# Optimization experiments

Measured on AMD Instinct MI355X. Metric: run time of the kernel, lower is better.

Reference implementation:

```python
import jax, jax.numpy as jnp
import numpy as np

N_NODES = 50000
NEG_SLOPE = 0.2  # PyG GATConv default leaky_relu slope
EPS = 1e-16      # PyG softmax denominator epsilon


def gat_layer(x, src, dst, W, a_src, a_dst, b):
    # x: [N, F_in], W: [F_in, H, F_out], a_*: [H, F_out], b: [F_out]
    h = jnp.einsum('ni,iho->nho', x, W)                      # [N, H, O]
    alpha_src = jnp.sum(h * a_src, axis=-1)                  # [N, H]
    alpha_dst = jnp.sum(h * a_dst, axis=-1)                  # [N, H]
    e = jax.nn.leaky_relu(alpha_src[src] + alpha_dst[dst], NEG_SLOPE)  # [E, H]
    # segment softmax over incoming edges of each destination node
    m = jax.ops.segment_max(e, dst, num_segments=N_NODES)   # [N, H]
    ex = jnp.exp(e - m[dst])
    s = jax.ops.segment_sum(ex, dst, num_segments=N_NODES)  # [N, H]
    alpha = ex / (s[dst] + EPS)                              # [E, H]
    out = jax.ops.segment_sum(alpha[:, :, None] * h[src], dst, num_segments=N_NODES)  # [N, H, O]
    out = out.mean(axis=1) + b                               # concat=False -> mean over heads
    return jax.nn.relu(out)                                  # norm=Identity, dropout p=0 no-op


def setup_inputs() -> dict:
    key = jax.random.key(0)
    ks = jax.random.split(key, 12)
    d = 64
    H = 4
    E = 800000
    inp = {
        'x': jax.random.normal(ks[0], (N_NODES, d), dtype=jnp.float32),
        'edge_index': jax.random.randint(ks[1], (2, E), 0, N_NODES, dtype=jnp.int64),
        'edge_attr': jax.random.normal(ks[2], (E, 8), dtype=jnp.float32),
        'dropout_rate': 0,
    }
    sc = 1.0 / np.sqrt(d)
    for li, base in ((1, 3), (2, 7)):
        inp[f'W{li}'] = jax.random.normal(ks[base], (d, H, d), dtype=jnp.float32) * sc
        inp[f'a_src{li}'] = jax.random.normal(ks[base + 1], (H, d), dtype=jnp.float32) * sc
        inp[f'a_dst{li}'] = jax.random.normal(ks[base + 2], (H, d), dtype=jnp.float32) * sc
        inp[f'b{li}'] = jnp.zeros((d,), dtype=jnp.float32)
    return inp


def reference(x, edge_index, edge_attr, dropout_rate,
              W1, a_src1, a_dst1, b1, W2, a_src2, a_dst2, b2):
    # edge_attr unused: GATConv built without edge_dim has no lin_edge.
    src, dst = edge_index[0], edge_index[1]
    x = gat_layer(x, src, dst, W1, a_src1, a_dst1, b1)
    x = gat_layer(x, src, dst, W2, a_src2, a_dst2, b2)
    return x
```

## Files before the change

### kernel.cpp

```cpp
#include <hip/hip_runtime.h>
#include <hip/hip_bf16.h>
#include <math.h>

#define N_NODES 50000
#define NEG_SLOPE 0.2f
#define EPS_DEN 1e-16f

#define NBUCK 196
#define NBLK  512

typedef float f4v __attribute__((ext_vector_type(4)));

__global__ void __launch_bounds__(256) prep_k(
    const float* __restrict__ W, const float* __restrict__ aS,
    const float* __restrict__ aD, float* __restrict__ WaSD)
{
    int tid = threadIdx.x;
    int h = tid >> 6, i = tid & 63;
    const float* wrow = W + (size_t)i * 256 + h * 64;
    const float* as = aS + h * 64;
    const float* ad = aD + h * 64;
    float ws = 0.f, wd = 0.f;
    #pragma unroll 8
    for (int o = 0; o < 64; ++o) {
        float w = wrow[o];
        ws = fmaf(w, as[o], ws);
        wd = fmaf(w, ad[o], wd);
    }
    WaSD[i * 8 + h]     = ws;
    WaSD[i * 8 + 4 + h] = wd;
}

__global__ void __launch_bounds__(256) alpha_k(
    const float* __restrict__ x, const float* __restrict__ WaSD,
    float* __restrict__ asrc, float* __restrict__ adst, int N)
{
    __shared__ float Wl[512];
    int tid = threadIdx.x;
    Wl[tid]       = WaSD[tid];
    Wl[tid + 256] = WaSD[tid + 256];
    __syncthreads();

    int node = blockIdx.x * 64 + (tid >> 2);
    int q = tid & 3;
    if (node >= N) return;

    float pS[4] = {0.f, 0.f, 0.f, 0.f};
    float pD[4] = {0.f, 0.f, 0.f, 0.f};
    const float* xp = x + (size_t)node * 64 + q * 16;
    #pragma unroll
    for (int j = 0; j < 4; ++j) {
        float4 xv = *(const float4*)(xp + j * 4);
        float xr[4] = {xv.x, xv.y, xv.z, xv.w};
        #pragma unroll
        for (int u = 0; u < 4; ++u) {
            int i = q * 16 + j * 4 + u;
            float4 wS = *(const float4*)(Wl + i * 8);
            float4 wD = *(const float4*)(Wl + i * 8 + 4);
            pS[0] = fmaf(xr[u], wS.x, pS[0]); pS[1] = fmaf(xr[u], wS.y, pS[1]);
            pS[2] = fmaf(xr[u], wS.z, pS[2]); pS[3] = fmaf(xr[u], wS.w, pS[3]);
            pD[0] = fmaf(xr[u], wD.x, pD[0]); pD[1] = fmaf(xr[u], wD.y, pD[1]);
            pD[2] = fmaf(xr[u], wD.z, pD[2]); pD[3] = fmaf(xr[u], wD.w, pD[3]);
        }
    }
    #pragma unroll
    for (int off = 1; off <= 2; off <<= 1) {
        #pragma unroll
        for (int h = 0; h < 4; ++h) {
            pS[h] += __shfl_xor(pS[h], off);
            pD[h] += __shfl_xor(pD[h], off);
        }
    }
    if (q == 0) {
        *(float4*)(asrc + 4 * (size_t)node) = make_float4(pS[0], pS[1], pS[2], pS[3]);
        *(float4*)(adst + 4 * (size_t)node) = make_float4(pD[0], pD[1], pD[2], pD[3]);
    }
}

__global__ void __launch_bounds__(256) hist_bucket_k(
    const int* __restrict__ ei, int* __restrict__ bh, int E)
{
    __shared__ int lh[NBUCK];
    int tid = threadIdx.x;
    for (int b = tid; b < NBUCK; b += 256) lh[b] = 0;
    __syncthreads();

    const int ch = (E + NBLK - 1) / NBLK;
    const int e0 = blockIdx.x * ch;
    const int e1 = min(e0 + ch, E);
    for (int e = e0 + tid; e < e1; e += 256)
        atomicAdd(&lh[ei[E + e] >> 8], 1);
    __syncthreads();
    for (int b = tid; b < NBUCK; b += 256)
        bh[(size_t)b * NBLK + blockIdx.x] = lh[b];
}

__global__ void __launch_bounds__(64) bscan_k(
    const int* __restrict__ bh, int* __restrict__ boffL, int* __restrict__ btot)
{
    const int b = blockIdx.x;
    const int lane = threadIdx.x;
    int v[8];
    int base = b * NBLK;
    #pragma unroll
    for (int u = 0; u < 8; ++u) v[u] = bh[base + lane * 8 + u];
    int t = 0;
    #pragma unroll
    for (int u = 0; u < 8; ++u) t += v[u];
    int run = t;
    #pragma unroll
    for (int off = 1; off < 64; off <<= 1) {
        int u = __shfl_up(run, off);
        if (lane >= off) run += u;
    }
    int lane_base = run - t;
    #pragma unroll
    for (int u = 0; u < 8; ++u) {
        boffL[base + lane * 8 + u] = lane_base;
        lane_base += v[u];
    }
    if (lane == 63) btot[b] = run;
}

__global__ void __launch_bounds__(256) btot_k(
    const int* __restrict__ btot, int* __restrict__ bbase,
    int* __restrict__ row, int N, int E)
{
    __shared__ int sd[256];
    int tid = threadIdx.x;
    int v = (tid < NBUCK) ? btot[tid] : 0;
    sd[tid] = v;
    __syncthreads();
    for (int off = 1; off < 256; off <<= 1) {
        int t = (tid >= off) ? sd[tid - off] : 0;
        __syncthreads();
        sd[tid] += t;
        __syncthreads();
    }
    if (tid < NBUCK) bbase[tid] = sd[tid] - v;
    if (tid == 0) { bbase[NBUCK] = E; row[N] = E; }
}

__global__ void __launch_bounds__(256) bplace_k(
    const int* __restrict__ ei, const int* __restrict__ bbase,
    const int* __restrict__ boffL, unsigned int* __restrict__ stage, int E)
{
    __shared__ int cur[NBUCK];
    int tid = threadIdx.x;
    for (int b = tid; b < NBUCK; b += 256)
        cur[b] = bbase[b] + boffL[(size_t)b * NBLK + blockIdx.x];
    __syncthreads();

    const int ch = (E + NBLK - 1) / NBLK;
    const int e0 = blockIdx.x * ch;
    const int e1 = min(e0 + ch, E);
    for (int e = e0 + tid; e < e1; e += 256) {
        int s = ei[e];
        int d = ei[E + e];
        int pos = atomicAdd(&cur[d >> 8], 1);
        stage[pos] = (unsigned int)s | ((unsigned int)(d & 255) << 16);
    }
}

__global__ void __launch_bounds__(256) bscatter_k(
    const unsigned int* __restrict__ stage, const int* __restrict__ bbase,
    int* __restrict__ row, int* __restrict__ psrc, int N)
{
    __shared__ int cnt[256];
    __shared__ int sd[256];
    __shared__ int cur[256];
    const int b = blockIdx.x;
    const int tid = threadIdx.x;
    const int nb0 = b << 8;
    const int es = bbase[b], ee = bbase[b + 1];

    cnt[tid] = 0;
    __syncthreads();
    for (int idx = es + tid; idx < ee; idx += 256)
        atomicAdd(&cnt[(stage[idx] >> 16) & 255], 1);
    __syncthreads();

    int v = cnt[tid];
    sd[tid] = v;
    __syncthreads();
    for (int off = 1; off < 256; off <<= 1) {
        int t = (tid >= off) ? sd[tid - off] : 0;
        __syncthreads();
        sd[tid] += t;
        __syncthreads();
    }
    int r = es + sd[tid] - v;
    int node = nb0 + tid;
    if (node < N) row[node] = r;
    cur[tid] = r;
    __syncthreads();

    for (int idx = es + tid; idx < ee; idx += 256) {
        unsigned int w = stage[idx];
        int pos = atomicAdd(&cur[(w >> 16) & 255], 1);
        psrc[pos] = w & 0xFFFF;
    }
}

#define MAXDEG4 64
__global__ void __launch_bounds__(256) aggzw_k(
    const float* __restrict__ x, const float* __restrict__ asrc,
    const float* __restrict__ adst, const int* __restrict__ row,
    const int* __restrict__ psrc, const float* __restrict__ W,
    const float* __restrict__ bias, float* __restrict__ out, int N)
{
    __shared__ float smem[9808];
    float4* pL = (float4*)smem;
    int*    sI = (int*)(smem + 4160);
    float*  zt = smem + 5200;
    float*  Wc = smem;
    float*  red = smem;

    const int tid  = threadIdx.x;
    const int lane = tid & 63;
    const int li   = lane & 15;
    const int slot = tid >> 4;
    const int n = blockIdx.x * 16 + slot;
    const bool active = n < N;

    int rs = 0, deg = 0;
    float4 ad = make_float4(0.f, 0.f, 0.f, 0.f);
    if (active) {
        rs  = row[n];
        deg = row[n + 1] - rs;
        ad  = *(const float4*)(adst + 4 * (size_t)n);
    }

    float m0 = -INFINITY, m1 = -INFINITY, m2 = -INFINITY, m3 = -INFINITY;
    float s0 = 0.f, s1 = 0.f, s2 = 0.f, s3 = 0.f;
    float4 a0 = make_float4(0.f,0.f,0.f,0.f), a1 = a0, a2 = a0, a3 = a0;
    const float* xb = x + (size_t)li * 4;

    if (deg <= MAXDEG4) {
        for (int j = li; j < deg; j += 16) {
            int s = psrc[rs + j];
            sI[slot * 65 + j] = s;
            float4 a = *(const float4*)(asrc + 4 * (size_t)s);
            float e0 = a.x + ad.x; e0 = e0 > 0.f ? e0 : NEG_SLOPE * e0;
            float e1 = a.y + ad.y; e1 = e1 > 0.f ? e1 : NEG_SLOPE * e1;
            float e2 = a.z + ad.z; e2 = e2 > 0.f ? e2 : NEG_SLOPE * e2;
            float e3 = a.w + ad.w; e3 = e3 > 0.f ? e3 : NEG_SLOPE * e3;
            pL[slot * 65 + j] = make_float4(e0, e1, e2, e3);
            m0 = fmaxf(m0, e0); m1 = fmaxf(m1, e1);
            m2 = fmaxf(m2, e2); m3 = fmaxf(m3, e3);
        }
        #pragma unroll
        for (int off = 1; off < 16; off <<= 1) {
            m0 = fmaxf(m0, __shfl_xor(m0, off));
            m1 = fmaxf(m1, __shfl_xor(m1, off));
            m2 = fmaxf(m2, __shfl_xor(m2, off));
            m3 = fmaxf(m3, __shfl_xor(m3, off));
        }
        for (int j = li; j < deg; j += 16) {
            float4 e = pL[slot * 65 + j];
            float4 p = make_float4(__expf(e.x - m0), __expf(e.y - m1),
                                   __expf(e.z - m2), __expf(e.w - m3));
            pL[slot * 65 + j] = p;
            s0 += p.x; s1 += p.y; s2 += p.z; s3 += p.w;
        }
        #pragma unroll
        for (int off = 1; off < 16; off <<= 1) {
            s0 += __shfl_xor(s0, off);
            s1 += __shfl_xor(s1, off);
            s2 += __shfl_xor(s2, off);
            s3 += __shfl_xor(s3, off);
        }
        #pragma unroll 2
        for (int j = 0; j < deg; ++j) {
            int s = sI[slot * 65 + j];
            float4 p = pL[slot * 65 + j];
            float4 xv = *(const float4*)(xb + (size_t)s * 64);
            a0.x = fmaf(p.x, xv.x, a0.x); a0.y = fmaf(p.x, xv.y, a0.y);
            a0.z = fmaf(p.x, xv.z, a0.z); a0.w = fmaf(p.x, xv.w, a0.w);
            a1.x = fmaf(p.y, xv.x, a1.x); a1.y = fmaf(p.y, xv.y, a1.y);
            a1.z = fmaf(p.y, xv.z, a1.z); a1.w = fmaf(p.y, xv.w, a1.w);
            a2.x = fmaf(p.z, xv.x, a2.x); a2.y = fmaf(p.z, xv.y, a2.y);
            a2.z = fmaf(p.z, xv.z, a2.z); a2.w = fmaf(p.z, xv.w, a2.w);
            a3.x = fmaf(p.w, xv.x, a3.x); a3.y = fmaf(p.w, xv.y, a3.y);
            a3.z = fmaf(p.w, xv.z, a3.z); a3.w = fmaf(p.w, xv.w, a3.w);
        }
    } else {
        for (int j = li; j < deg; j += 16) {
            int s = psrc[rs + j];
            float4 a = *(const float4*)(asrc + 4 * (size_t)s);
            float e0 = a.x + ad.x; e0 = e0 > 0.f ? e0 : NEG_SLOPE * e0;
            float e1 = a.y + ad.y; e1 = e1 > 0.f ? e1 : NEG_SLOPE * e1;
            float e2 = a.z + ad.z; e2 = e2 > 0.f ? e2 : NEG_SLOPE * e2;
            float e3 = a.w + ad.w; e3 = e3 > 0.f ? e3 : NEG_SLOPE * e3;
            m0 = fmaxf(m0, e0); m1 = fmaxf(m1, e1);
            m2 = fmaxf(m2, e2); m3 = fmaxf(m3, e3);
        }
        #pragma unroll
        for (int off = 1; off < 16; off <<= 1) {
            m0 = fmaxf(m0, __shfl_xor(m0, off));
            m1 = fmaxf(m1, __shfl_xor(m1, off));
            m2 = fmaxf(m2, __shfl_xor(m2, off));
            m3 = fmaxf(m3, __shfl_xor(m3, off));
        }
        for (int j = li; j < deg; j += 16) {
            int s = psrc[rs + j];
            float4 a = *(const float4*)(asrc + 4 * (size_t)s);
            float e0 = a.x + ad.x; e0 = e0 > 0.f ? e0 : NEG_SLOPE * e0;
            float e1 = a.y + ad.y; e1 = e1 > 0.f ? e1 : NEG_SLOPE * e1;
            float e2 = a.z + ad.z; e2 = e2 > 0.f ? e2 : NEG_SLOPE * e2;
            float e3 = a.w + ad.w; e3 = e3 > 0.f ? e3 : NEG_SLOPE * e3;
            s0 += __expf(e0 - m0); s1 += __expf(e1 - m1);
            s2 += __expf(e2 - m2); s3 += __expf(e3 - m3);
        }
        #pragma unroll
        for (int off = 1; off < 16; off <<= 1) {
            s0 += __shfl_xor(s0, off);
            s1 += __shfl_xor(s1, off);
            s2 += __shfl_xor(s2, off);
            s3 += __shfl_xor(s3, off);
        }
        for (int j = 0; j < deg; ++j) {
            int s = psrc[rs + j];
            float4 a = *(const float4*)(asrc + 4 * (size_t)s);
            float e0 = a.x + ad.x; e0 = e0 > 0.f ? e0 : NEG_SLOPE * e0;
            float e1 = a.y + ad.y; e1 = e1 > 0.f ? e1 : NEG_SLOPE * e1;
            float e2 = a.z + ad.z; e2 = e2 > 0.f ? e2 : NEG_SLOPE * e2;
            float e3 = a.w + ad.w; e3 = e3 > 0.f ? e3 : NEG_SLOPE * e3;
            float p0 = __expf(e0 - m0), p1 = __expf(e1 - m1);
            float p2 = __expf(e2 - m2), p3 = __expf(e3 - m3);
            float4 xv = *(const float4*)(xb + (size_t)s * 64);
            a0.x = fmaf(p0, xv.x, a0.x); a0.y = fmaf(p0, xv.y, a0.y);
            a0.z = fmaf(p0, xv.z, a0.z); a0.w = fmaf(p0, xv.w, a0.w);
            a1.x = fmaf(p1, xv.x, a1.x); a1.y = fmaf(p1, xv.y, a1.y);
            a1.z = fmaf(p1, xv.z, a1.z); a1.w = fmaf(p1, xv.w, a1.w);
            a2.x = fmaf(p2, xv.x, a2.x); a2.y = fmaf(p2, xv.y, a2.y);
            a2.z = fmaf(p2, xv.z, a2.z); a2.w = fmaf(p2, xv.w, a2.w);
            a3.x = fmaf(p3, xv.x, a3.x); a3.y = fmaf(p3, xv.y, a3.y);
            a3.z = fmaf(p3, xv.z, a3.z); a3.w = fmaf(p3, xv.w, a3.w);
        }
    }

    if (active) {
        float i0 = 0.25f / (s0 + EPS_DEN), i1 = 0.25f / (s1 + EPS_DEN);
        float i2 = 0.25f / (s2 + EPS_DEN), i3 = 0.25f / (s3 + EPS_DEN);
        float vh[4][4] = {
            {a0.x * i0, a0.y * i0, a0.z * i0, a0.w * i0},
            {a1.x * i1, a1.y * i1, a1.z * i1, a1.w * i1},
            {a2.x * i2, a2.y * i2, a2.z * i2, a2.w * i2},
            {a3.x * i3, a3.y * i3, a3.z * i3, a3.w * i3}
        };
        #pragma unroll
        for (int h = 0; h < 4; ++h)
            #pragma unroll
            for (int u = 0; u < 4; ++u)
                zt[(h * 64 + li * 4 + u) * 18 + slot] = vh[h][u];
    }

    const int ks = tid >> 6;
    const int ng = (tid >> 4) & 3;
    const int og = tid & 15;
    float acc[4][4];
    #pragma unroll
    for (int i = 0; i < 4; ++i)
        #pragma unroll
        for (int j = 0; j < 4; ++j) acc[i][j] = 0.f;

    for (int cc = 0; cc < 4; ++cc) {
        __syncthreads();
        #pragma unroll
        for (int it = 0; it < 4; ++it) {
            int idx = tid + 256 * it;
            int k   = idx >> 4;
            int o4  = (idx & 15) << 2;
            *(float4*)(Wc + k * 64 + o4) =
                *(const float4*)(W + (size_t)k * 256 + cc * 64 + o4);
        }
        __syncthreads();

        #pragma unroll
        for (int kk = 0; kk < 16; ++kk) {
            int kl = ks * 16 + kk;
            int kg = cc * 64 + kl;
            float2 zA = *(const float2*)(zt + kg * 18 + ng * 4);
            float2 zB = *(const float2*)(zt + kg * 18 + ng * 4 + 2);
            float4 wv = *(const float4*)(Wc + kl * 64 + og * 4);
            float zr[4] = {zA.x, zA.y, zB.x, zB.y};
            float wc4[4] = {wv.x, wv.y, wv.z, wv.w};
            #pragma unroll
            for (int i = 0; i < 4; ++i)
                #pragma unroll
                for (int j = 0; j < 4; ++j)
                    acc[i][j] = fmaf(zr[i], wc4[j], acc[i][j]);
        }
    }

    __syncthreads();
    #pragma unroll
    for (int i = 0; i < 4; ++i)
        *(float4*)(red + ((ks * 16 + ng * 4 + i) * 16 + og) * 4) =
            make_float4(acc[i][0], acc[i][1], acc[i][2], acc[i][3]);
    __syncthreads();

    {
        int nl = tid >> 4;
        int o  = tid & 15;
        const float4* r4 = (const float4*)red;
        float4 p0 = r4[      nl * 16 + o];
        float4 p1 = r4[256 + nl * 16 + o];
        float4 p2 = r4[512 + nl * 16 + o];
        float4 p3 = r4[768 + nl * 16 + o];
        int gn = blockIdx.x * 16 + nl;
        if (gn < N) {
            float4 b4 = *(const float4*)(bias + o * 4);
            float4 ov;
            ov.x = fmaxf(p0.x + p1.x + p2.x + p3.x + b4.x, 0.f);
            ov.y = fmaxf(p0.y + p1.y + p2.y + p3.y + b4.y, 0.f);
            ov.z = fmaxf(p0.z + p1.z + p2.z + p3.z + b4.z, 0.f);
            ov.w = fmaxf(p0.w + p1.w + p2.w + p3.w + b4.w, 0.f);
            *(float4*)(out + (size_t)gn * 64 + o * 4) = ov;
        }
    }
}

extern "C" void kernel_launch(void* const* d_in, const int* in_sizes, int n_in,
                              void* d_out, int out_size, void* d_ws, size_t ws_size,
                              hipStream_t stream)
{
    const float* x   = (const float*)d_in[0];
    const int*   ei  = (const int*)d_in[1];
    const float* W1  = (const float*)d_in[4];
    const float* as1 = (const float*)d_in[5];
    const float* ad1 = (const float*)d_in[6];
    const float* b1  = (const float*)d_in[7];
    const float* W2  = (const float*)d_in[8];
    const float* as2 = (const float*)d_in[9];
    const float* ad2 = (const float*)d_in[10];
    const float* b2  = (const float*)d_in[11];

    const int E = in_sizes[1] / 2;
    const int N = N_NODES;

    char* ws = (char*)d_ws;
    size_t off = 0;
    auto alloc = [&](size_t bytes) -> void* {
        void* p = ws + off;
        off = (off + bytes + 255) & ~(size_t)255;
        return p;
    };
    float*        x1    = (float*)alloc((size_t)N * 64 * 4);
    float*        asrc  = (float*)alloc((size_t)N * 4 * 4);
    float*        adst  = (float*)alloc((size_t)N * 4 * 4);
    float*        WaSD  = (float*)alloc(64 * 8 * 4);
    int*          row   = (int*)alloc((size_t)(N + 1) * 4);
    int*          psrc  = (int*)alloc((size_t)E * 4);
    int*          bh    = (int*)alloc((size_t)NBUCK * NBLK * 4);
    int*          boffL = (int*)alloc((size_t)NBUCK * NBLK * 4);
    int*          btot  = (int*)alloc((NBUCK + 1) * 4);
    int*          bbase = (int*)alloc((NBUCK + 1) * 4);
    unsigned int* stage = (unsigned int*)alloc((size_t)E * 4);

    hist_bucket_k<<<NBLK, 256, 0, stream>>>(ei, bh, E);
    bscan_k<<<NBUCK, 64, 0, stream>>>(bh, boffL, btot);
    btot_k<<<1, 256, 0, stream>>>(btot, bbase, row, N, E);
    bplace_k<<<NBLK, 256, 0, stream>>>(ei, bbase, boffL, stage, E);
    bscatter_k<<<NBUCK, 256, 0, stream>>>(stage, bbase, row, psrc, N);

    const int nblk64 = (N + 63) / 64;
    const int nblk16 = (N + 15) / 16;

    prep_k<<<1, 256, 0, stream>>>(W1, as1, ad1, WaSD);
    alpha_k<<<nblk64, 256, 0, stream>>>(x, WaSD, asrc, adst, N);
    aggzw_k<<<nblk16, 256, 0, stream>>>(x, asrc, adst, row, psrc, W1, b1, x1, N);

    prep_k<<<1, 256, 0, stream>>>(W2, as2, ad2, WaSD);
    alpha_k<<<nblk64, 256, 0, stream>>>(x1, WaSD, asrc, adst, N);
    aggzw_k<<<nblk16, 256, 0, stream>>>(x1, asrc, adst, row, psrc, W2, b2, (float*)d_out, N);
}
```

Baseline: 190.2 us.

## Shrink aggregation LDS footprint, read W from global, raise occupancy

Shared memory in the fused aggregate-and-transform kernel drops from about 39KB to 20KB. The per-slot source index cache is removed so indices are re-read from psrc, and the staged W chunks are replaced by direct global float4 loads of W inside the transform loop, which also removes the per-chunk barriers. The z tile is re-laid out with stride 20 so it can be read as float4, and launch bounds request 8 blocks per CU. In exchange, W and psrc now come through cache instead of LDS, and the register budget tightens, which could cause spills.

```diff
diff --git a/kernel.cpp b/kernel.cpp
--- a/kernel.cpp
+++ b/kernel.cpp
@@ -203,22 +203,19 @@
 }
 
 #define MAXDEG4 64
-__global__ void __launch_bounds__(256) aggzw_k(
+__global__ void __launch_bounds__(256, 8) aggzw_k(
     const float* __restrict__ x, const float* __restrict__ asrc,
     const float* __restrict__ adst, const int* __restrict__ row,
     const int* __restrict__ psrc, const float* __restrict__ W,
     const float* __restrict__ bias, float* __restrict__ out, int N)
 {
-    __shared__ float smem[9808];
+    __shared__ float smem[5120];
     float4* pL = (float4*)smem;
-    int*    sI = (int*)(smem + 4160);
-    float*  zt = smem + 5200;
-    float*  Wc = smem;
+    float*  zt = smem;
     float*  red = smem;
 
     const int tid  = threadIdx.x;
-    const int lane = tid & 63;
-    const int li   = lane & 15;
+    const int li   = tid & 15;
     const int slot = tid >> 4;
     const int n = blockIdx.x * 16 + slot;
     const bool active = n < N;
@@ -234,12 +231,10 @@
     float m0 = -INFINITY, m1 = -INFINITY, m2 = -INFINITY, m3 = -INFINITY;
     float s0 = 0.f, s1 = 0.f, s2 = 0.f, s3 = 0.f;
     float4 a0 = make_float4(0.f,0.f,0.f,0.f), a1 = a0, a2 = a0, a3 = a0;
-    const float* xb = x + (size_t)li * 4;
 
     if (deg <= MAXDEG4) {
         for (int j = li; j < deg; j += 16) {
             int s = psrc[rs + j];
-            sI[slot * 65 + j] = s;
             float4 a = *(const float4*)(asrc + 4 * (size_t)s);
             float e0 = a.x + ad.x; e0 = e0 > 0.f ? e0 : NEG_SLOPE * e0;
             float e1 = a.y + ad.y; e1 = e1 > 0.f ? e1 : NEG_SLOPE * e1;
@@ -272,9 +267,9 @@
         }
         #pragma unroll 2
         for (int j = 0; j < deg; ++j) {
-            int s = sI[slot * 65 + j];
+            int s = psrc[rs + j];
             float4 p = pL[slot * 65 + j];
-            float4 xv = *(const float4*)(xb + (size_t)s * 64);
+            float4 xv = *(const float4*)(x + (size_t)s * 64 + li * 4);
             a0.x = fmaf(p.x, xv.x, a0.x); a0.y = fmaf(p.x, xv.y, a0.y);
             a0.z = fmaf(p.x, xv.z, a0.z); a0.w = fmaf(p.x, xv.w, a0.w);
             a1.x = fmaf(p.y, xv.x, a1.x); a1.y = fmaf(p.y, xv.y, a1.y);
@@ -328,7 +323,7 @@
             float e3 = a.w + ad.w; e3 = e3 > 0.f ? e3 : NEG_SLOPE * e3;
             float p0 = __expf(e0 - m0), p1 = __expf(e1 - m1);
             float p2 = __expf(e2 - m2), p3 = __expf(e3 - m3);
-            float4 xv = *(const float4*)(xb + (size_t)s * 64);
+            float4 xv = *(const float4*)(x + (size_t)s * 64 + li * 4);
             a0.x = fmaf(p0, xv.x, a0.x); a0.y = fmaf(p0, xv.y, a0.y);
             a0.z = fmaf(p0, xv.z, a0.z); a0.w = fmaf(p0, xv.w, a0.w);
             a1.x = fmaf(p1, xv.x, a1.x); a1.y = fmaf(p1, xv.y, a1.y);
@@ -340,21 +335,20 @@
         }
     }
 
+    __syncthreads();
     if (active) {
         float i0 = 0.25f / (s0 + EPS_DEN), i1 = 0.25f / (s1 + EPS_DEN);
         float i2 = 0.25f / (s2 + EPS_DEN), i3 = 0.25f / (s3 + EPS_DEN);
-        float vh[4][4] = {
-            {a0.x * i0, a0.y * i0, a0.z * i0, a0.w * i0},
-            {a1.x * i1, a1.y * i1, a1.z * i1, a1.w * i1},
-            {a2.x * i2, a2.y * i2, a2.z * i2, a2.w * i2},
-            {a3.x * i3, a3.y * i3, a3.z * i3, a3.w * i3}
-        };
-        #pragma unroll
-        for (int h = 0; h < 4; ++h)
-            #pragma unroll
-            for (int u = 0; u < 4; ++u)
-                zt[(h * 64 + li * 4 + u) * 18 + slot] = vh[h][u];
-    }
+        float* zb = zt + (li * 4) * 20 + slot;
+        zb[0]  = a0.x * i0; zb[20] = a0.y * i0; zb[40] = a0.z * i0; zb[60] = a0.w * i0;
+        zb += 64 * 20;
+        zb[0]  = a1.x * i1; zb[20] = a1.y * i1; zb[40] = a1.z * i1; zb[60] = a1.w * i1;
+        zb += 64 * 20;
+        zb[0]  = a2.x * i2; zb[20] = a2.y * i2; zb[40] = a2.z * i2; zb[60] = a2.w * i2;
+        zb += 64 * 20;
+        zb[0]  = a3.x * i3; zb[20] = a3.y * i3; zb[40] = a3.z * i3; zb[60] = a3.w * i3;
+    }
+    __syncthreads();
 
     const int ks = tid >> 6;
     const int ng = (tid >> 4) & 3;
@@ -365,33 +359,19 @@
         #pragma unroll
         for (int j = 0; j < 4; ++j) acc[i][j] = 0.f;
 
-    for (int cc = 0; cc < 4; ++cc) {
-        __syncthreads();
-        #pragma unroll
-        for (int it = 0; it < 4; ++it) {
-            int idx = tid + 256 * it;
-            int k   = idx >> 4;
-            int o4  = (idx & 15) << 2;
-            *(float4*)(Wc + k * 64 + o4) =
-                *(const float4*)(W + (size_t)k * 256 + cc * 64 + o4);
-        }
-        __syncthreads();
-
-        #pragma unroll
-        for (int kk = 0; kk < 16; ++kk) {
-            int kl = ks * 16 + kk;
-            int kg = cc * 64 + kl;
-            float2 zA = *(const float2*)(zt + kg * 18 + ng * 4);
-            float2 zB = *(const float2*)(zt + kg * 18 + ng * 4 + 2);
-            float4 wv = *(const float4*)(Wc + kl * 64 + og * 4);
-            float zr[4] = {zA.x, zA.y, zB.x, zB.y};
-            float wc4[4] = {wv.x, wv.y, wv.z, wv.w};
+    const float* wp = W + (size_t)ks * 64 + og * 4;
+    #pragma unroll 8
+    for (int kk = 0; kk < 64; ++kk) {
+        int kg = ks * 64 + kk;
+        float4 zv = *(const float4*)(zt + kg * 20 + ng * 4);
+        float4 wv = *(const float4*)(wp + (size_t)kk * 256);
+        float zr[4] = {zv.x, zv.y, zv.z, zv.w};
+        float wc4[4] = {wv.x, wv.y, wv.z, wv.w};
+        #pragma unroll
+        for (int i = 0; i < 4; ++i)
             #pragma unroll
-            for (int i = 0; i < 4; ++i)
-                #pragma unroll
-                for (int j = 0; j < 4; ++j)
-                    acc[i][j] = fmaf(zr[i], wc4[j], acc[i][j]);
-        }
+            for (int j = 0; j < 4; ++j)
+                acc[i][j] = fmaf(zr[i], wc4[j], acc[i][j]);
     }
 
     __syncthreads();
```

Measured after the change: 186.1 us. -2.1%, faster.
